# Kernel optimization log

Hardware: AMD Instinct MI355X
Metric: run time of the kernel (lower is better)

Reference implementation:

```python
import jax, jax.numpy as jnp
import numpy as np

B, R, T = 16, 400, 400   # batch, ROIs, BOLD length (= feature_nums)
H, Q = 8, 64             # heads, per-head dim
K_DIL = 4                # dilated_parameter_k
N_GCN = 8


def setup_inputs() -> dict:
    key = jax.random.key(0)
    ks = jax.random.split(key, 12)
    s = lambda *sh: 1.0 / np.sqrt(sh[0])
    return {
        "x": jax.random.normal(ks[0], (B, R, T), jnp.float32),
        "Wk": jax.random.normal(ks[1], (T, H * Q), jnp.float32) * s(T),
        "bk": jnp.zeros((H * Q,), jnp.float32),
        "se_W1": jax.random.normal(ks[2], (H, H // 2), jnp.float32) * s(H),
        "se_b1": jnp.zeros((H // 2,), jnp.float32),
        "se_W2": jax.random.normal(ks[3], (H // 2, H), jnp.float32) * s(H // 2),
        "se_b2": jnp.zeros((H,), jnp.float32),
        "gcn_W": jax.random.normal(ks[4], (N_GCN, T, T), jnp.float32) * s(T),
        "gcn_b": jnp.zeros((N_GCN, T), jnp.float32),
        "fuse_w": jax.random.normal(ks[5], (H,), jnp.float32) * s(H),
        "fuse_b": jnp.zeros((), jnp.float32),
        "mlp_W1": jax.random.normal(ks[6], (T, 256), jnp.float32) * s(T),
        "mlp_b1": jnp.zeros((256,), jnp.float32),
        "mlp_W2": jax.random.normal(ks[7], (256, 128), jnp.float32) * s(256),
        "mlp_b2": jnp.zeros((128,), jnp.float32),
        "mlp_W3": jax.random.normal(ks[8], (128, 64), jnp.float32) * s(128),
        "mlp_b3": jnp.zeros((64,), jnp.float32),
        "mlp_W4": jax.random.normal(ks[9], (64, 5), jnp.float32) * s(64),
        "mlp_b4": jnp.zeros((5,), jnp.float32),
    }


def reference(x, Wk, bk, se_W1, se_b1, se_W2, se_b2, gcn_W, gcn_b,
              fuse_w, fuse_b, mlp_W1, mlp_b1, mlp_W2, mlp_b2,
              mlp_W3, mlp_b3, mlp_W4, mlp_b4):
    dt = x.dtype
    # ---- Transformer: Q = K = linear_k(x) (as in source) ----
    qk = (x @ Wk + bk).reshape(B, R, H, Q).transpose(0, 2, 1, 3)  # [B,H,R,Q]
    rel = jnp.einsum('bhrq,bhsq->bhrs', qk, qk) / jnp.sqrt(jnp.asarray(Q, dt))
    rel = jax.nn.softmax(jax.nn.relu(rel), axis=-1)               # [B,H,R,R]
    # ---- SE gate over heads ----
    gap = rel.mean(axis=(2, 3))                                   # [B,H]
    gate = jax.nn.sigmoid(jax.nn.relu(gap @ se_W1 + se_b1) @ se_W2 + se_b2)
    rel = rel * gate[:, :, None, None]
    # ---- dilated mask (deterministic prob<0.8 branch) ----
    idx = jnp.argsort(rel, axis=-1)                               # [B,H,R,R]
    sel = (idx == 0) | ((idx >= 2 ** K_DIL) & (idx < 2 ** K_DIL + 5))
    mask = jnp.minimum(sel.astype(dt) + jnp.eye(R, dtype=dt), 1.0)
    adj = rel * mask                                              # [B,H,R,R]
    feats = jnp.broadcast_to(x[:, None], (B, H, R, T))            # [B,H,R,T]
    for i in range(N_GCN):
        msg = jnp.einsum('bhrs,bhst->bhrt', adj, feats)
        feats = jax.nn.relu(msg @ gcn_W[i] + gcn_b[i]) + feats
    # ---- 1x1 conv fusion over heads ----
    fused = jnp.einsum('bhrt,h->brt', feats, fuse_w) + fuse_b     # [B,R,T]
    # ---- MLP head ----
    h = jax.nn.relu(fused @ mlp_W1 + mlp_b1)
    h = jax.nn.relu(h @ mlp_W2 + mlp_b2)
    h = jax.nn.relu(h @ mlp_W3 + mlp_b3)
    return jax.nn.relu(h @ mlp_W4 + mlp_b4)                       # [B,R,5]
```

## Files before the change

### kernel.cpp

```cpp
#include <hip/hip_runtime.h>
#include <math.h>

namespace {

constexpr int nB = 16, nR = 400, nT = 400, nH = 8, nQ = 64;
constexpr int BH = nB * nH;
constexpr int HQ = nH * nQ;
constexpr int KP = 416;
constexpr int NK = KP / 32;

typedef __attribute__((ext_vector_type(8))) short short8;
typedef __attribute__((ext_vector_type(4))) float floatx4;

__device__ __forceinline__ unsigned short f2bf(float f) {
  unsigned int u = __float_as_uint(f);
  unsigned int r = (u + 0x7fffu + ((u >> 16) & 1u)) >> 16;
  return (unsigned short)r;
}
__device__ __forceinline__ float bf2f(unsigned short u) {
  return __uint_as_float(((unsigned int)u) << 16);
}

__device__ __forceinline__ void dma16(const void* g, void* l) {
  __builtin_amdgcn_global_load_lds(
      (const __attribute__((address_space(1))) unsigned int*)g,
      (__attribute__((address_space(3))) unsigned int*)l, 16, 0, 0);
}

template<int BM, int BN, int BK, int TM, int TN, bool RELU>
__global__ __launch_bounds__(256) void gemm_k(
    const float* __restrict__ A, const float* __restrict__ W,
    const float* __restrict__ bias,
    float* C, int M, int N, int K)
{
  constexpr int NT = (BM / TM) * (BN / TN);
  static_assert(NT == 256, "block must be 256 threads");
  __shared__ float As[BK][BM + 4];
  __shared__ float Bs[BK][BN + 4];
  const int tid = threadIdx.x;
  const int bm = blockIdx.y * BM;
  const int bn = blockIdx.x * BN;
  const int tx = tid % (BN / TN);
  const int ty = tid / (BN / TN);
  const bool n4ok = ((N & 3) == 0);

  float acc[TM][TN];
#pragma unroll
  for (int i = 0; i < TM; ++i)
#pragma unroll
    for (int j = 0; j < TN; ++j) acc[i][j] = 0.f;

  for (int kt = 0; kt < K; kt += BK) {
#pragma unroll
    for (int i = 0; i < (BM * BK) / (NT * 4); ++i) {
      int flat = (tid + i * NT) * 4;
      int m = flat / BK;
      int k = flat % BK;
      float4 v = *(const float4*)(A + (size_t)(bm + m) * K + kt + k);
      As[k + 0][m] = v.x; As[k + 1][m] = v.y;
      As[k + 2][m] = v.z; As[k + 3][m] = v.w;
    }
#pragma unroll
    for (int i = 0; i < (BK * BN) / (NT * 4); ++i) {
      int flat = (tid + i * NT) * 4;
      int k = flat / BN;
      int n = flat % BN;
      int gn = bn + n;
      float4 v;
      if (n4ok && gn + 3 < N) {
        v = *(const float4*)(W + (size_t)(kt + k) * N + gn);
      } else {
        v.x = (gn + 0 < N) ? W[(size_t)(kt + k) * N + gn + 0] : 0.f;
        v.y = (gn + 1 < N) ? W[(size_t)(kt + k) * N + gn + 1] : 0.f;
        v.z = (gn + 2 < N) ? W[(size_t)(kt + k) * N + gn + 2] : 0.f;
        v.w = (gn + 3 < N) ? W[(size_t)(kt + k) * N + gn + 3] : 0.f;
      }
      *(float4*)&Bs[k][n] = v;
    }
    __syncthreads();
#pragma unroll
    for (int k = 0; k < BK; ++k) {
      float a[TM], b[TN];
#pragma unroll
      for (int i = 0; i < TM; i += 4)
        *(float4*)&a[i] = *(const float4*)&As[k][ty * TM + i];
#pragma unroll
      for (int j = 0; j < TN; j += 4)
        *(float4*)&b[j] = *(const float4*)&Bs[k][tx * TN + j];
#pragma unroll
      for (int i = 0; i < TM; ++i)
#pragma unroll
        for (int j = 0; j < TN; ++j) acc[i][j] += a[i] * b[j];
    }
    __syncthreads();
  }

#pragma unroll
  for (int i = 0; i < TM; ++i) {
    const int gm = bm + ty * TM + i;
    float* crow = C + (size_t)gm * N;
#pragma unroll
    for (int j = 0; j < TN; j += 4) {
      const int gn = bn + tx * TN + j;
      if (n4ok && gn + 3 < N) {
        float4 bv = *(const float4*)(bias + gn);
        float4 v;
        v.x = acc[i][j + 0] + bv.x; v.y = acc[i][j + 1] + bv.y;
        v.z = acc[i][j + 2] + bv.z; v.w = acc[i][j + 3] + bv.w;
        if (RELU) {
          v.x = fmaxf(v.x, 0.f); v.y = fmaxf(v.y, 0.f);
          v.z = fmaxf(v.z, 0.f); v.w = fmaxf(v.w, 0.f);
        }
        *(float4*)(crow + gn) = v;
      } else {
#pragma unroll
        for (int jj = 0; jj < 4; ++jj) {
          int gnn = gn + jj;
          if (gnn < N) {
            float v = acc[i][j + jj] + bias[gnn];
            if (RELU) v = fmaxf(v, 0.f);
            crow[gnn] = v;
          }
        }
      }
    }
  }
}

__global__ void xsplit_k(const float* __restrict__ x,
                         unsigned short* __restrict__ xh,
                         unsigned short* __restrict__ xl)
{
  int i = blockIdx.x * 256 + threadIdx.x;
  constexpr int total = 6400 * (KP / 4);
  if (i >= total) return;
  int row = i / (KP / 4), cg = i - row * (KP / 4);
  int c = cg * 4;
  ushort4 h = make_ushort4(0, 0, 0, 0), l = make_ushort4(0, 0, 0, 0);
  if (c < 400) {
    float4 v = *(const float4*)(x + (size_t)row * 400 + c);
    h.x = f2bf(v.x); l.x = f2bf(v.x - bf2f(h.x));
    h.y = f2bf(v.y); l.y = f2bf(v.y - bf2f(h.y));
    h.z = f2bf(v.z); l.z = f2bf(v.z - bf2f(h.z));
    h.w = f2bf(v.w); l.w = f2bf(v.w - bf2f(h.w));
  }
  *(ushort4*)(xh + (size_t)row * KP + c) = h;
  *(ushort4*)(xl + (size_t)row * KP + c) = l;
}

__global__ void hfx_k(const unsigned short* __restrict__ feats,
                      const float* __restrict__ fw, const float* __restrict__ fb,
                      unsigned short* __restrict__ xh,
                      unsigned short* __restrict__ xl)
{
  int i = blockIdx.x * 256 + threadIdx.x;
  constexpr int total = 6400 * (KP / 4);
  if (i >= total) return;
  int row = i / (KP / 4), cg = i - row * (KP / 4);
  int c = cg * 4;
  ushort4 h = make_ushort4(0, 0, 0, 0), l = make_ushort4(0, 0, 0, 0);
  if (c < 400) {
    const int bb = row / nR;
    const int r = row - bb * nR;
    float fbv = fb[0];
    float4 acc = {fbv, fbv, fbv, fbv};
#pragma unroll
    for (int hh = 0; hh < nH; ++hh) {
      float w = fw[hh];
      ushort4 v = *(const ushort4*)(feats +
          (((size_t)(bb * nH + hh) * nR + r) * nT + c));
      acc.x += w * bf2f(v.x); acc.y += w * bf2f(v.y);
      acc.z += w * bf2f(v.z); acc.w += w * bf2f(v.w);
    }
    h.x = f2bf(acc.x); l.x = f2bf(acc.x - bf2f(h.x));
    h.y = f2bf(acc.y); l.y = f2bf(acc.y - bf2f(h.y));
    h.z = f2bf(acc.z); l.z = f2bf(acc.z - bf2f(h.z));
    h.w = f2bf(acc.w); l.w = f2bf(acc.w - bf2f(h.w));
  }
  *(ushort4*)(xh + (size_t)row * KP + c) = h;
  *(ushort4*)(xl + (size_t)row * KP + c) = l;
}

__global__ void wksplit_k(const float* __restrict__ W, int N,
                          unsigned short* __restrict__ Wth,
                          unsigned short* __restrict__ Wtl)
{
  __shared__ float t[32][33];
  const int k0 = blockIdx.x * 32;
  const int n0 = blockIdx.y * 32;
  const int tx = threadIdx.x, ty = threadIdx.y;
#pragma unroll
  for (int r = 0; r < 32; r += 8) {
    int k = k0 + ty + r, n = n0 + tx;
    t[ty + r][tx] = (k < 400) ? W[(size_t)k * N + n] : 0.f;
  }
  __syncthreads();
#pragma unroll
  for (int r = 0; r < 32; r += 8) {
    int n = n0 + ty + r, k = k0 + tx;
    float v = t[tx][ty + r];
    unsigned short h = f2bf(v);
    Wth[(size_t)n * KP + k] = h;
    Wtl[(size_t)n * KP + k] = f2bf(v - bf2f(h));
  }
}

template<bool RELU>
__global__ __launch_bounds__(256) void sgemm_mfma(
    const unsigned short* __restrict__ Ah, const unsigned short* __restrict__ Al,
    const unsigned short* __restrict__ Bh, const unsigned short* __restrict__ Bl,
    const float* __restrict__ bias,
    float* __restrict__ C, int N)
{
  __shared__ __align__(16) char smem[49152];

  const int tid = threadIdx.x;
  const int lane = tid & 63;
  const int wave = tid >> 6;

  const int bm = blockIdx.y * 64;
  const int bn = blockIdx.x * 64;

  const int wm = (wave & 1) * 32;
  const int wn = (wave >> 1) * 32;

  const unsigned short* kbase = (wave == 0) ? Ah : (wave == 1) ? Al
                              : (wave == 2) ? Bh : Bl;
  const int rbase0 = (wave < 2) ? bm : bn;
  const unsigned short* gsrc[4];
  int goff[4];
#pragma unroll
  for (int j = 0; j < 4; ++j) {
    const int row = rbase0 + j * 16 + (lane & 15);
    gsrc[j] = kbase + (size_t)row * KP + (lane >> 4) * 8;
    goff[j] = (wave * 4 + j) * 1024;
  }

#pragma unroll
  for (int j = 0; j < 4; ++j) dma16(gsrc[j], smem + goff[j]);
#pragma unroll
  for (int j = 0; j < 4; ++j) dma16(gsrc[j] + 32, smem + 16384 + goff[j]);

  floatx4 acc[2][2] = {};
  const int ao = (wm >> 4) * 1024;
  const int bo = (wn >> 4) * 1024;
  const int lb = lane * 16;

#pragma unroll
  for (int k = 0; k < NK; ++k) {
    if (k == NK - 1)
      asm volatile("s_waitcnt vmcnt(0)" ::: "memory");
    else
      asm volatile("s_waitcnt vmcnt(4)" ::: "memory");
    __builtin_amdgcn_s_barrier();
    __builtin_amdgcn_sched_barrier(0);
    if (k + 2 < NK) {
      char* dst = smem + ((k + 2) % 3) * 16384;
#pragma unroll
      for (int j = 0; j < 4; ++j)
        dma16(gsrc[j] + (k + 2) * 32, dst + goff[j]);
    }
    const char* base = smem + (k % 3) * 16384;
    short8 ah[2], al[2], bh[2], bl[2];
#pragma unroll
    for (int mi = 0; mi < 2; ++mi) {
      ah[mi] = *(const short8*)(base + ao + mi * 1024 + lb);
      al[mi] = *(const short8*)(base + 4096 + ao + mi * 1024 + lb);
    }
#pragma unroll
    for (int ni = 0; ni < 2; ++ni) {
      bh[ni] = *(const short8*)(base + 8192 + bo + ni * 1024 + lb);
      bl[ni] = *(const short8*)(base + 12288 + bo + ni * 1024 + lb);
    }
#pragma unroll
    for (int mi = 0; mi < 2; ++mi)
#pragma unroll
      for (int ni = 0; ni < 2; ++ni) {
        acc[mi][ni] = __builtin_amdgcn_mfma_f32_16x16x32_bf16(
            ah[mi], bh[ni], acc[mi][ni], 0, 0, 0);
        acc[mi][ni] = __builtin_amdgcn_mfma_f32_16x16x32_bf16(
            ah[mi], bl[ni], acc[mi][ni], 0, 0, 0);
        acc[mi][ni] = __builtin_amdgcn_mfma_f32_16x16x32_bf16(
            al[mi], bh[ni], acc[mi][ni], 0, 0, 0);
      }
  }

  float* Os = (float*)smem;
  __syncthreads();
#pragma unroll
  for (int mi = 0; mi < 2; ++mi)
#pragma unroll
    for (int ni = 0; ni < 2; ++ni)
#pragma unroll
      for (int r = 0; r < 4; ++r) {
        const int lrow = wm + mi * 16 + (lane >> 4) * 4 + r;
        const int cl = wn + ni * 16 + (lane & 15);
        Os[lrow * 68 + cl] = acc[mi][ni][r];
      }
  __syncthreads();

#pragma unroll
  for (int ii = 0; ii < 4; ++ii) {
    const int f = tid + ii * 256;
    const int row = f >> 4;
    const int c4 = (f & 15) << 2;
    float4 v = *(const float4*)&Os[row * 68 + c4];
    float4 bb = *(const float4*)(bias + bn + c4);
    v.x += bb.x; v.y += bb.y; v.z += bb.z; v.w += bb.w;
    if (RELU) {
      v.x = fmaxf(v.x, 0.f); v.y = fmaxf(v.y, 0.f);
      v.z = fmaxf(v.z, 0.f); v.w = fmaxf(v.w, 0.f);
    }
    *(float4*)(C + (size_t)(bm + row) * N + bn + c4) = v;
  }
}

__global__ __launch_bounds__(256) void gcn_gemm(
    const unsigned short* __restrict__ A,
    const unsigned short* __restrict__ Bt,
    const float* __restrict__ bias,
    unsigned short* __restrict__ Cb,
    const float* __restrict__ x, int first)
{
  __shared__ __align__(16) char smem[36864];

  const int tid = threadIdx.x;
  const int lane = tid & 63;
  const int wave = tid >> 6;

  const int b = blockIdx.x;
  const int xcd = b & 7;
  const int s = b >> 3;
  const int loc = s / 7;
  const int nt = s - loc * 7;
  const int mt = loc * 8 + xcd;
  const int bm = mt * 128;
  const int bn = nt * 64;

  const int wm = (wave & 1) * 64;
  const int wn = (wave >> 1) * 32;

  const unsigned short* gsrc[3];
  int goff[3];
#pragma unroll
  for (int j = 0; j < 3; ++j) {
    const int g = wave * 3 + j;
    if (g < 8) {
      const int row = bm + g * 16 + (lane & 15);
      gsrc[j] = A + (size_t)row * KP + (lane >> 4) * 8;
      goff[j] = g * 1024;
    } else {
      int row = bn + (g - 8) * 16 + (lane & 15);
      if (row > 415) row = 415;
      gsrc[j] = Bt + (size_t)row * KP + (lane >> 4) * 8;
      goff[j] = 8192 + (g - 8) * 1024;
    }
  }

  const int rcol = bn + ((tid & 15) << 2);
  ushort4 resv[2][4];
  if (!first && rcol < nT) {
#pragma unroll
    for (int rh = 0; rh < 2; ++rh)
#pragma unroll
      for (int ii = 0; ii < 4; ++ii) {
        const int gr = bm + rh * 64 + (tid >> 4) + ii * 16;
        resv[rh][ii] = *(const ushort4*)(Cb + (size_t)gr * nT + rcol);
      }
  }

#pragma unroll
  for (int j = 0; j < 3; ++j)
    dma16(gsrc[j], smem + goff[j]);
#pragma unroll
  for (int j = 0; j < 3; ++j)
    dma16(gsrc[j] + 32, smem + 12288 + goff[j]);

  floatx4 acc[4][2] = {};
  const int aoff = (wm >> 4) * 1024;
  const int boff = 8192 + (wn >> 4) * 1024;
  const int lb = lane * 16;

#pragma unroll
  for (int k = 0; k < NK; ++k) {
    if (k == NK - 1)
      asm volatile("s_waitcnt vmcnt(0)" ::: "memory");
    else
      asm volatile("s_waitcnt vmcnt(3)" ::: "memory");
    __builtin_amdgcn_s_barrier();
    __builtin_amdgcn_sched_barrier(0);
    if (k + 2 < NK) {
      char* dst = smem + ((k + 2) % 3) * 12288;
#pragma unroll
      for (int j = 0; j < 3; ++j)
        dma16(gsrc[j] + (k + 2) * 32, dst + goff[j]);
    }
    const char* base = smem + (k % 3) * 12288;
    short8 av[4], bv[2];
#pragma unroll
    for (int mi = 0; mi < 4; ++mi)
      av[mi] = *(const short8*)(base + aoff + mi * 1024 + lb);
#pragma unroll
    for (int ni = 0; ni < 2; ++ni)
      bv[ni] = *(const short8*)(base + boff + ni * 1024 + lb);
#pragma unroll
    for (int mi = 0; mi < 4; ++mi)
#pragma unroll
      for (int ni = 0; ni < 2; ++ni)
        acc[mi][ni] = __builtin_amdgcn_mfma_f32_16x16x32_bf16(
            av[mi], bv[ni], acc[mi][ni], 0, 0, 0);
  }

  float bvv[2];
#pragma unroll
  for (int ni = 0; ni < 2; ++ni) {
    const int col = bn + wn + ni * 16 + (lane & 15);
    bvv[ni] = (col < nT) ? bias[col] : 0.f;
  }

  float* Os = (float*)smem;

  __syncthreads();
#pragma unroll
  for (int mi = 0; mi < 4; ++mi)
#pragma unroll
    for (int ni = 0; ni < 2; ++ni)
#pragma unroll
      for (int r = 0; r < 4; ++r) {
        const int lrow = wm + mi * 16 + (lane >> 4) * 4 + r;
        const int cl = wn + ni * 16 + (lane & 15);
        Os[lrow * 68 + cl] = fmaxf(acc[mi][ni][r] + bvv[ni], 0.f);
      }
  __syncthreads();

#pragma unroll
  for (int ii = 0; ii < 8; ++ii) {
    const int f = tid + ii * 256;
    const int row = f >> 4;
    const int c4 = (f & 15) << 2;
    const int col = bn + c4;
    if (col < nT) {
      const int gr = bm + row;
      float4 v = *(const float4*)&Os[row * 68 + c4];
      float r0, r1, r2, r3;
      if (first) {
        const int bh = gr / nR;
        const int rr = gr - bh * nR;
        const float* rrow = x + (size_t)(bh >> 3) * (nR * nT) + (size_t)rr * nT;
        float4 rv = *(const float4*)(rrow + col);
        r0 = rv.x; r1 = rv.y; r2 = rv.z; r3 = rv.w;
      } else {
        ushort4 rv = resv[ii >> 2][ii & 3];
        r0 = bf2f(rv.x); r1 = bf2f(rv.y); r2 = bf2f(rv.z); r3 = bf2f(rv.w);
      }
      ushort4 o;
      o.x = f2bf(v.x + r0); o.y = f2bf(v.y + r1);
      o.z = f2bf(v.z + r2); o.w = f2bf(v.w + r3);
      *(ushort4*)(Cb + (size_t)gr * nT + col) = o;
    }
  }
}

__global__ void wprep_k(const float* __restrict__ W, unsigned short* __restrict__ Wt)
{
  __shared__ float t[32][33];
  const int i = blockIdx.z;
  const int k0 = blockIdx.x * 32;
  const int n0 = blockIdx.y * 32;
  const int tx = threadIdx.x, ty = threadIdx.y;
#pragma unroll
  for (int r = 0; r < 32; r += 8) {
    int k = k0 + ty + r, n = n0 + tx;
    t[ty + r][tx] = (k < nT && n < nT) ? W[(size_t)i * nT * nT + (size_t)k * nT + n] : 0.f;
  }
  __syncthreads();
#pragma unroll
  for (int r = 0; r < 32; r += 8) {
    int n = n0 + ty + r, k = k0 + tx;
    Wt[(size_t)i * KP * KP + (size_t)n * KP + k] = f2bf(t[tx][ty + r]);
  }
}

__global__ void gate_k(const float* __restrict__ w1, const float* __restrict__ b1,
                       const float* __restrict__ w2, const float* __restrict__ b2,
                       float* gate)
{
  if (threadIdx.x == 0 && blockIdx.x == 0) {
    float h1[4];
    const float gap = 1.0f / 400.0f;
#pragma unroll
    for (int i = 0; i < 4; ++i) {
      float s = b1[i];
      for (int h = 0; h < 8; ++h) s += gap * w1[h * 4 + i];
      h1[i] = fmaxf(s, 0.f);
    }
#pragma unroll
    for (int h = 0; h < 8; ++h) {
      float s = b2[h];
      for (int i = 0; i < 4; ++i) s += h1[i] * w2[i * 8 + h];
      gate[h] = 1.f / (1.f + expf(-s));
    }
  }
}

__global__ __launch_bounds__(256) void qkscore_k(
    const float* __restrict__ qk, float* __restrict__ sc)
{
  __shared__ float Qs[64][68];
  __shared__ float Ks[64][68];

  const int tm = blockIdx.y;
  const int tn = blockIdx.x;
  if (tm > tn) return;

  const int tid = threadIdx.x;
  const int bh = blockIdx.z;
  const int b = bh >> 3, h = bh & 7;
  const int bm = tm * 64;
  const int bn = tn * 64;
  const float* qkb = qk + (size_t)b * nR * HQ + h * nQ;

  {
    const int row = tid & 63;
#pragma unroll
    for (int p = 0; p < 4; ++p) {
      const int kc = (tid >> 6) + p * 4;
      int gr = bm + row; if (gr > 399) gr = 399;
      float4 v = *(const float4*)(qkb + (size_t)gr * HQ + (kc << 2));
      Qs[kc * 4 + 0][row] = v.x; Qs[kc * 4 + 1][row] = v.y;
      Qs[kc * 4 + 2][row] = v.z; Qs[kc * 4 + 3][row] = v.w;
      int gs2 = bn + row; if (gs2 > 399) gs2 = 399;
      float4 w = *(const float4*)(qkb + (size_t)gs2 * HQ + (kc << 2));
      Ks[kc * 4 + 0][row] = w.x; Ks[kc * 4 + 1][row] = w.y;
      Ks[kc * 4 + 2][row] = w.z; Ks[kc * 4 + 3][row] = w.w;
    }
  }
  __syncthreads();

  const int tx = tid & 15;
  const int ty = tid >> 4;
  float acc[4][4] = {};
#pragma unroll 8
  for (int k = 0; k < 64; ++k) {
    float4 a = *(const float4*)&Qs[k][ty * 4];
    float4 bv = *(const float4*)&Ks[k][tx * 4];
    acc[0][0] += a.x * bv.x; acc[0][1] += a.x * bv.y; acc[0][2] += a.x * bv.z; acc[0][3] += a.x * bv.w;
    acc[1][0] += a.y * bv.x; acc[1][1] += a.y * bv.y; acc[1][2] += a.y * bv.z; acc[1][3] += a.y * bv.w;
    acc[2][0] += a.z * bv.x; acc[2][1] += a.z * bv.y; acc[2][2] += a.z * bv.z; acc[2][3] += a.z * bv.w;
    acc[3][0] += a.w * bv.x; acc[3][1] += a.w * bv.y; acc[3][2] += a.w * bv.z; acc[3][3] += a.w * bv.w;
  }

  float* scb = sc + (size_t)bh * nR * 400;

  {
    const int gc = bn + tx * 4;
    if (gc < 400) {
#pragma unroll
      for (int i = 0; i < 4; ++i) {
        const int gr = bm + ty * 4 + i;
        if (gr < 400) {
          float4 o;
          o.x = fmaxf(acc[i][0] * 0.125f, 0.f);
          o.y = fmaxf(acc[i][1] * 0.125f, 0.f);
          o.z = fmaxf(acc[i][2] * 0.125f, 0.f);
          o.w = fmaxf(acc[i][3] * 0.125f, 0.f);
          *(float4*)(scb + (size_t)gr * 400 + gc) = o;
        }
      }
    }
  }

  if (tm != tn) {
    const int gc = bm + ty * 4;
    if (gc < 400) {
#pragma unroll
      for (int j = 0; j < 4; ++j) {
        const int gr = bn + tx * 4 + j;
        if (gr < 400) {
          float4 o;
          o.x = fmaxf(acc[0][j] * 0.125f, 0.f);
          o.y = fmaxf(acc[1][j] * 0.125f, 0.f);
          o.z = fmaxf(acc[2][j] * 0.125f, 0.f);
          o.w = fmaxf(acc[3][j] * 0.125f, 0.f);
          *(float4*)(scb + (size_t)gr * 400 + gc) = o;
        }
      }
    }
  }
}

__global__ __launch_bounds__(256) void rankadj_k(
    const float* __restrict__ sc, const float* __restrict__ gate,
    float* __restrict__ adjval, int* __restrict__ adjcol)
{
  __shared__ float rowbuf[4][408];

  const int wave = threadIdx.x >> 6;
  const int lane = threadIdx.x & 63;
  const int row = blockIdx.x * 4 + wave;
  const int bh = row / nR;
  const int r = row - bh * nR;
  const float* srow = sc + (size_t)row * 400;

  float v[7];
  bool valid[7];
#pragma unroll
  for (int it = 0; it < 7; ++it) {
    const int j = lane + it * 64;
    valid[it] = (j < 400);
    v[it] = valid[it] ? srow[j] : 0.f;
  }

  float m = 0.f;
#pragma unroll
  for (int it = 0; it < 7; ++it) m = fmaxf(m, v[it]);
#pragma unroll
  for (int o = 32; o > 0; o >>= 1) m = fmaxf(m, __shfl_xor(m, o));

  float e[7];
  float s = 0.f;
#pragma unroll
  for (int it = 0; it < 7; ++it) {
    e[it] = valid[it] ? expf(v[it] - m) : 0.f;
    s += e[it];
  }
#pragma unroll
  for (int o = 32; o > 0; o >>= 1) s += __shfl_xor(s, o);

  const float g = gate[bh & 7];
  float val[7];
#pragma unroll
  for (int it = 0; it < 7; ++it) val[it] = (e[it] / s) * g;

#pragma unroll
  for (int it = 0; it < 7; ++it)
    if (valid[it]) rowbuf[wave][lane + it * 64] = val[it];
  __syncthreads();

  const int csp[6] = {0, 16, 17, 18, 19, 20};
  float vc[6];
#pragma unroll
  for (int i = 0; i < 6; ++i) vc[i] = rowbuf[wave][csp[i]];
  int rk[6] = {0, 0, 0, 0, 0, 0};
#pragma unroll
  for (int it = 0; it < 7; ++it) {
    if (valid[it]) {
      const int j = lane + it * 64;
      const float vj = val[it];
#pragma unroll
      for (int i = 0; i < 6; ++i)
        rk[i] += (vj < vc[i]) ? 1 : ((vj == vc[i] && j < csp[i]) ? 1 : 0);
    }
  }
#pragma unroll
  for (int i = 0; i < 6; ++i)
#pragma unroll
    for (int o = 32; o > 0; o >>= 1) rk[i] += __shfl_xor(rk[i], o);

  if (lane == 0) {
    const size_t base = (size_t)row * 8;
    bool dup = false;
#pragma unroll
    for (int i = 0; i < 6; ++i) {
      const int p = rk[i];
      adjcol[base + i] = p;
      adjval[base + i] = rowbuf[wave][p];
      dup = dup || (p == r);
    }
    adjcol[base + 6] = r;
    adjval[base + 6] = dup ? 0.f : rowbuf[wave][r];
    adjcol[base + 7] = r;
    adjval[base + 7] = 0.f;
  }
}

__global__ __launch_bounds__(256) void spmsg_k(
    const int* __restrict__ adjcol, const float* __restrict__ adjval,
    const unsigned short* __restrict__ feats, const float* __restrict__ x,
    int first, unsigned short* __restrict__ msg)
{
  __shared__ unsigned short fs[400 * 36];

  const int tid = threadIdx.x;
  const int bh = blockIdx.x;
  const int c0 = blockIdx.y * 32;

  if (first) {
    const float* src = x + (size_t)(bh >> 3) * (nR * nT);
    for (int i = tid; i < 1600; i += 256) {
      const int r = i >> 2, g = i & 3;
      const int c = c0 + g * 8;
      ushort4 lo = make_ushort4(0, 0, 0, 0), hi = make_ushort4(0, 0, 0, 0);
      if (c < 400) {
        float4 v0 = *(const float4*)(src + (size_t)r * nT + c);
        float4 v1 = *(const float4*)(src + (size_t)r * nT + c + 4);
        lo = make_ushort4(f2bf(v0.x), f2bf(v0.y), f2bf(v0.z), f2bf(v0.w));
        hi = make_ushort4(f2bf(v1.x), f2bf(v1.y), f2bf(v1.z), f2bf(v1.w));
      }
      *(ushort4*)&fs[r * 36 + g * 8] = lo;
      *(ushort4*)&fs[r * 36 + g * 8 + 4] = hi;
    }
  } else {
    const unsigned short* src = feats + (size_t)bh * nR * nT;
    for (int i = tid; i < 1600; i += 256) {
      const int r = i >> 2, g = i & 3;
      const int c = c0 + g * 8;
      short8 v = {};
      if (c < 400) v = *(const short8*)(src + (size_t)r * nT + c);
      *(short8*)&fs[r * 36 + g * 8] = v;
    }
  }
  __syncthreads();

  const int* ac = adjcol + (size_t)bh * nR * 8;
  const float* av = adjval + (size_t)bh * nR * 8;
  for (int i = tid; i < 1600; i += 256) {
    const int r = i >> 2, g = i & 3;
    const int c = c0 + g * 8;
    unsigned short* o = msg + ((size_t)bh * nR + r) * KP + c;
    if (c >= 400) {
      short8 z = {};
      *(short8*)o = z;
      continue;
    }
    int4 c03 = *(const int4*)(ac + r * 8);
    int4 c47 = *(const int4*)(ac + r * 8 + 4);
    float4 v03 = *(const float4*)(av + r * 8);
    float4 v47 = *(const float4*)(av + r * 8 + 4);
    const int col[7] = {c03.x, c03.y, c03.z, c03.w, c47.x, c47.y, c47.z};
    const float val[7] = {v03.x, v03.y, v03.z, v03.w, v47.x, v47.y, v47.z};
    float a[8] = {};
#pragma unroll
    for (int j = 0; j < 7; ++j) {
      short8 v = *(const short8*)&fs[col[j] * 36 + g * 8];
      const float w = val[j];
#pragma unroll
      for (int e = 0; e < 8; ++e)
        a[e] += w * bf2f((unsigned short)v[e]);
    }
    short8 ov;
#pragma unroll
    for (int e = 0; e < 8; ++e) ov[e] = (short)f2bf(a[e]);
    *(short8*)o = ov;
  }
}

}

extern "C" void kernel_launch(void* const* d_in, const int* in_sizes, int n_in,
                              void* d_out, int out_size, void* d_ws, size_t ws_size,
                              hipStream_t stream)
{
  (void)in_sizes; (void)n_in; (void)out_size; (void)ws_size;
  const float* x    = (const float*)d_in[0];
  const float* Wk   = (const float*)d_in[1];
  const float* bk   = (const float*)d_in[2];
  const float* seW1 = (const float*)d_in[3];
  const float* seb1 = (const float*)d_in[4];
  const float* seW2 = (const float*)d_in[5];
  const float* seb2 = (const float*)d_in[6];
  const float* gcnW = (const float*)d_in[7];
  const float* gcnb = (const float*)d_in[8];
  const float* fw   = (const float*)d_in[9];
  const float* fb   = (const float*)d_in[10];
  const float* mW1  = (const float*)d_in[11];
  const float* mb1  = (const float*)d_in[12];
  const float* mW2  = (const float*)d_in[13];
  const float* mb2  = (const float*)d_in[14];
  const float* mW3  = (const float*)d_in[15];
  const float* mb3  = (const float*)d_in[16];
  const float* mW4  = (const float*)d_in[17];
  const float* mb4  = (const float*)d_in[18];
  float* out = (float*)d_out;

  float* ws     = (float*)d_ws;
  float* adjval = ws;
  int*   adjcol = (int*)(adjval + 409600);
  float* gate   = (float*)(adjcol + 409600);
  unsigned short* Wt = (unsigned short*)(gate + 64);
  float* qk     = gate + 64 + 692224;
  float* region = qk + (size_t)3276800;
  float* scores = region;
  unsigned short* featsb = (unsigned short*)region;
  unsigned short* msg = (unsigned short*)(region + 10240000);

  unsigned short* xh  = (unsigned short*)region;
  unsigned short* xl  = xh + (size_t)6400 * KP;
  unsigned short* Wth = xl + (size_t)6400 * KP;
  unsigned short* Wtl = Wth + (size_t)512 * KP;

  unsigned short* mxh  = (unsigned short*)msg;
  unsigned short* mxl  = mxh + (size_t)6400 * KP;
  unsigned short* mWth = mxl + (size_t)6400 * KP;
  unsigned short* mWtl = mWth + (size_t)256 * KP;
  float* h1 = (float*)(mWtl + (size_t)256 * KP);
  float* h2 = h1 + (size_t)6400 * 256;
  float* h3 = h2 + (size_t)6400 * 128;

  wprep_k<<<dim3(13, 13, 8), dim3(32, 8), 0, stream>>>(gcnW, Wt);

  xsplit_k<<<2600, 256, 0, stream>>>(x, xh, xl);
  wksplit_k<<<dim3(13, 16), dim3(32, 8), 0, stream>>>(Wk, 512, Wth, Wtl);
  sgemm_mfma<false><<<dim3(8, 100), 256, 0, stream>>>(
      xh, xl, Wth, Wtl, bk, qk, 512);

  gate_k<<<1, 64, 0, stream>>>(seW1, seb1, seW2, seb2, gate);

  qkscore_k<<<dim3(7, 7, 128), 256, 0, stream>>>(qk, scores);

  rankadj_k<<<12800, 256, 0, stream>>>(scores, gate, adjval, adjcol);

  for (int i = 0; i < 8; ++i) {
    const int first = (i == 0) ? 1 : 0;
    spmsg_k<<<dim3(BH, 13), 256, 0, stream>>>(adjcol, adjval, featsb, x,
                                              first, msg);
    gcn_gemm<<<dim3(2800), 256, 0, stream>>>(
        msg, Wt + (size_t)i * KP * KP, gcnb + (size_t)i * nT, featsb, x, first);
  }

  hfx_k<<<2600, 256, 0, stream>>>(featsb, fw, fb, mxh, mxl);

  wksplit_k<<<dim3(13, 8), dim3(32, 8), 0, stream>>>(mW1, 256, mWth, mWtl);
  sgemm_mfma<true><<<dim3(4, 100), 256, 0, stream>>>(
      mxh, mxl, mWth, mWtl, mb1, h1, 256);

  gemm_k<64, 64, 16, 4, 4, true><<<dim3(2, 100), 256, 0, stream>>>(
      h1, mW2, mb2, h2, 6400, 128, 256);
  gemm_k<64, 64, 16, 4, 4, true><<<dim3(1, 100), 256, 0, stream>>>(
      h2, mW3, mb3, h3, 6400, 64, 128);
  gemm_k<64, 64, 16, 4, 4, true><<<dim3(1, 100), 256, 0, stream>>>(
      h3, mW4, mb4, out, 6400, 5, 64);
}
```

Baseline: 786.4 us.

## Run MLP layers 2-3 on split-bf16 MFMA GEMM and widen spmsg per-thread work

Generalizes the split-bf16 MFMA GEMM over the K dimension and adds an option to emit hi/lo bf16 outputs directly. MLP layer 1 now writes split bf16, so layers 2 and 3 can use the MFMA kernel instead of the scalar fp32 gemm_k. Separately, each spmsg thread now handles 16 columns instead of 8, reusing the adjacency index loads. This adds small weight-split launches and more per-thread registers. The MLP layers are tiny compared with the GCN loop, so the overall effect is bounded.

After: 824.2 us. +4.8%, slower.

```diff
diff --git a/kernel.cpp b/kernel.cpp
--- a/kernel.cpp
+++ b/kernel.cpp
@@ -181,7 +181,7 @@
   *(ushort4*)(xl + (size_t)row * KP + c) = l;
 }
 
-__global__ void wksplit_k(const float* __restrict__ W, int N,
+__global__ void wksplit_k(const float* __restrict__ W, int K, int N, int KPo,
                           unsigned short* __restrict__ Wth,
                           unsigned short* __restrict__ Wtl)
 {
@@ -192,7 +192,7 @@
 #pragma unroll
   for (int r = 0; r < 32; r += 8) {
     int k = k0 + ty + r, n = n0 + tx;
-    t[ty + r][tx] = (k < 400) ? W[(size_t)k * N + n] : 0.f;
+    t[ty + r][tx] = (k < K) ? W[(size_t)k * N + n] : 0.f;
   }
   __syncthreads();
 #pragma unroll
@@ -200,18 +200,20 @@
     int n = n0 + ty + r, k = k0 + tx;
     float v = t[tx][ty + r];
     unsigned short h = f2bf(v);
-    Wth[(size_t)n * KP + k] = h;
-    Wtl[(size_t)n * KP + k] = f2bf(v - bf2f(h));
-  }
-}
-
-template<bool RELU>
+    Wth[(size_t)n * KPo + k] = h;
+    Wtl[(size_t)n * KPo + k] = f2bf(v - bf2f(h));
+  }
+}
+
+template<int NKt, bool RELU, bool OSPLIT>
 __global__ __launch_bounds__(256) void sgemm_mfma(
     const unsigned short* __restrict__ Ah, const unsigned short* __restrict__ Al,
     const unsigned short* __restrict__ Bh, const unsigned short* __restrict__ Bl,
     const float* __restrict__ bias,
-    float* __restrict__ C, int N)
-{
+    float* __restrict__ C, unsigned short* __restrict__ Ch,
+    unsigned short* __restrict__ Cl, int N)
+{
+  constexpr int KA = NKt * 32;
   __shared__ __align__(16) char smem[49152];
 
   const int tid = threadIdx.x;
@@ -232,7 +234,7 @@
 #pragma unroll
   for (int j = 0; j < 4; ++j) {
     const int row = rbase0 + j * 16 + (lane & 15);
-    gsrc[j] = kbase + (size_t)row * KP + (lane >> 4) * 8;
+    gsrc[j] = kbase + (size_t)row * KA + (lane >> 4) * 8;
     goff[j] = (wave * 4 + j) * 1024;
   }
 
@@ -247,14 +249,14 @@
   const int lb = lane * 16;
 
 #pragma unroll
-  for (int k = 0; k < NK; ++k) {
-    if (k == NK - 1)
+  for (int k = 0; k < NKt; ++k) {
+    if (k == NKt - 1)
       asm volatile("s_waitcnt vmcnt(0)" ::: "memory");
     else
       asm volatile("s_waitcnt vmcnt(4)" ::: "memory");
     __builtin_amdgcn_s_barrier();
     __builtin_amdgcn_sched_barrier(0);
-    if (k + 2 < NK) {
+    if (k + 2 < NKt) {
       char* dst = smem + ((k + 2) % 3) * 16384;
 #pragma unroll
       for (int j = 0; j < 4; ++j)
@@ -311,7 +313,17 @@
       v.x = fmaxf(v.x, 0.f); v.y = fmaxf(v.y, 0.f);
       v.z = fmaxf(v.z, 0.f); v.w = fmaxf(v.w, 0.f);
     }
-    *(float4*)(C + (size_t)(bm + row) * N + bn + c4) = v;
+    if (OSPLIT) {
+      ushort4 h, l;
+      h.x = f2bf(v.x); l.x = f2bf(v.x - bf2f(h.x));
+      h.y = f2bf(v.y); l.y = f2bf(v.y - bf2f(h.y));
+      h.z = f2bf(v.z); l.z = f2bf(v.z - bf2f(h.z));
+      h.w = f2bf(v.w); l.w = f2bf(v.w - bf2f(h.w));
+      *(ushort4*)(Ch + (size_t)(bm + row) * N + bn + c4) = h;
+      *(ushort4*)(Cl + (size_t)(bm + row) * N + bn + c4) = l;
+    } else {
+      *(float4*)(C + (size_t)(bm + row) * N + bn + c4) = v;
+    }
   }
 }
 
@@ -714,13 +726,14 @@
 
   const int* ac = adjcol + (size_t)bh * nR * 8;
   const float* av = adjval + (size_t)bh * nR * 8;
-  for (int i = tid; i < 1600; i += 256) {
-    const int r = i >> 2, g = i & 3;
-    const int c = c0 + g * 8;
+  for (int i = tid; i < 800; i += 256) {
+    const int r = i >> 1, g2 = i & 1;
+    const int c = c0 + g2 * 16;
     unsigned short* o = msg + ((size_t)bh * nR + r) * KP + c;
     if (c >= 400) {
       short8 z = {};
       *(short8*)o = z;
+      *(short8*)(o + 8) = z;
       continue;
     }
     int4 c03 = *(const int4*)(ac + r * 8);
@@ -729,19 +742,27 @@
     float4 v47 = *(const float4*)(av + r * 8 + 4);
     const int col[7] = {c03.x, c03.y, c03.z, c03.w, c47.x, c47.y, c47.z};
     const float val[7] = {v03.x, v03.y, v03.z, v03.w, v47.x, v47.y, v47.z};
-    float a[8] = {};
+    float a[16] = {};
 #pragma unroll
     for (int j = 0; j < 7; ++j) {
-      short8 v = *(const short8*)&fs[col[j] * 36 + g * 8];
+      const int fb = col[j] * 36 + g2 * 16;
+      short8 v0 = *(const short8*)&fs[fb];
+      short8 v1 = *(const short8*)&fs[fb + 8];
       const float w = val[j];
 #pragma unroll
-      for (int e = 0; e < 8; ++e)
-        a[e] += w * bf2f((unsigned short)v[e]);
-    }
-    short8 ov;
-#pragma unroll
-    for (int e = 0; e < 8; ++e) ov[e] = (short)f2bf(a[e]);
-    *(short8*)o = ov;
+      for (int e = 0; e < 8; ++e) {
+        a[e] += w * bf2f((unsigned short)v0[e]);
+        a[e + 8] += w * bf2f((unsigned short)v1[e]);
+      }
+    }
+    short8 ov0, ov1;
+#pragma unroll
+    for (int e = 0; e < 8; ++e) {
+      ov0[e] = (short)f2bf(a[e]);
+      ov1[e] = (short)f2bf(a[e + 8]);
+    }
+    *(short8*)o = ov0;
+    *(short8*)(o + 8) = ov1;
   }
 }
 
@@ -793,16 +814,22 @@
   unsigned short* mxl  = mxh + (size_t)6400 * KP;
   unsigned short* mWth = mxl + (size_t)6400 * KP;
   unsigned short* mWtl = mWth + (size_t)256 * KP;
-  float* h1 = (float*)(mWtl + (size_t)256 * KP);
-  float* h2 = h1 + (size_t)6400 * 256;
-  float* h3 = h2 + (size_t)6400 * 128;
+  unsigned short* h1h  = mWtl + (size_t)256 * KP;
+  unsigned short* h1l  = h1h + (size_t)6400 * 256;
+  unsigned short* w2h  = h1l + (size_t)6400 * 256;
+  unsigned short* w2l  = w2h + (size_t)128 * 256;
+  unsigned short* h2h  = w2l + (size_t)128 * 256;
+  unsigned short* h2l  = h2h + (size_t)6400 * 128;
+  unsigned short* w3h  = h2l + (size_t)6400 * 128;
+  unsigned short* w3l  = w3h + (size_t)64 * 128;
+  float* h3 = (float*)(w3l + (size_t)64 * 128 + 64);
 
   wprep_k<<<dim3(13, 13, 8), dim3(32, 8), 0, stream>>>(gcnW, Wt);
 
   xsplit_k<<<2600, 256, 0, stream>>>(x, xh, xl);
-  wksplit_k<<<dim3(13, 16), dim3(32, 8), 0, stream>>>(Wk, 512, Wth, Wtl);
-  sgemm_mfma<false><<<dim3(8, 100), 256, 0, stream>>>(
-      xh, xl, Wth, Wtl, bk, qk, 512);
+  wksplit_k<<<dim3(13, 16), dim3(32, 8), 0, stream>>>(Wk, 400, 512, 416, Wth, Wtl);
+  sgemm_mfma<13, false, false><<<dim3(8, 100), 256, 0, stream>>>(
+      xh, xl, Wth, Wtl, bk, qk, nullptr, nullptr, 512);
 
   gate_k<<<1, 64, 0, stream>>>(seW1, seb1, seW2, seb2, gate);
 
@@ -820,14 +847,18 @@
 
   hfx_k<<<2600, 256, 0, stream>>>(featsb, fw, fb, mxh, mxl);
 
-  wksplit_k<<<dim3(13, 8), dim3(32, 8), 0, stream>>>(mW1, 256, mWth, mWtl);
-  sgemm_mfma<true><<<dim3(4, 100), 256, 0, stream>>>(
-      mxh, mxl, mWth, mWtl, mb1, h1, 256);
-
-  gemm_k<64, 64, 16, 4, 4, true><<<dim3(2, 100), 256, 0, stream>>>(
-      h1, mW2, mb2, h2, 6400, 128, 256);
-  gemm_k<64, 64, 16, 4, 4, true><<<dim3(1, 100), 256, 0, stream>>>(
-      h2, mW3, mb3, h3, 6400, 64, 128);
+  wksplit_k<<<dim3(13, 8), dim3(32, 8), 0, stream>>>(mW1, 400, 256, 416, mWth, mWtl);
+  sgemm_mfma<13, true, true><<<dim3(4, 100), 256, 0, stream>>>(
+      mxh, mxl, mWth, mWtl, mb1, nullptr, h1h, h1l, 256);
+
+  wksplit_k<<<dim3(8, 4), dim3(32, 8), 0, stream>>>(mW2, 256, 128, 256, w2h, w2l);
+  sgemm_mfma<8, true, true><<<dim3(2, 100), 256, 0, stream>>>(
+      h1h, h1l, w2h, w2l, mb2, nullptr, h2h, h2l, 128);
+
+  wksplit_k<<<dim3(4, 2), dim3(32, 8), 0, stream>>>(mW3, 128, 64, 128, w3h, w3l);
+  sgemm_mfma<4, true, false><<<dim3(1, 100), 256, 0, stream>>>(
+      h2h, h2l, w3h, w3l, mb3, h3, nullptr, nullptr, 64);
+
   gemm_k<64, 64, 16, 4, 4, true><<<dim3(1, 100), 256, 0, stream>>>(
       h3, mW4, mb4, out, 6400, 5, 64);
 }
```
